# Performance work log

Measured on AMD Instinct MI355X. Metric: run time of the kernel, lower is better.

Reference implementation:

```python
import jax, jax.numpy as jnp
import numpy as np
import math

NUM_SECTORS = 8
HIDDEN = 128
FEAT = 64
MAX_DIST = 10.0


def gru_last(x, Wih, Whh, bih, bhh):
    # PyTorch GRU (gate order r,z,n); x: (B,T,D) -> last hidden (B,H)
    B = x.shape[0]
    H = Whh.shape[1]
    xp = jnp.einsum('btd,gd->btg', x, Wih) + bih  # (B,T,3H)

    def step(h, xpt):
        hp = h @ Whh.T + bhh
        xr, xz, xn = jnp.split(xpt, 3, -1)
        hr, hz, hn = jnp.split(hp, 3, -1)
        r = jax.nn.sigmoid(xr + hr)
        z = jax.nn.sigmoid(xz + hz)
        n = jnp.tanh(xn + r * hn)
        h_new = (1.0 - z) * n + z * h
        return h_new, None

    h0 = jnp.zeros((B, H), x.dtype)
    hT, _ = jax.lax.scan(step, h0, jnp.swapaxes(xp, 0, 1))
    return hT


def setup_inputs() -> dict:
    key = jax.random.key(0)
    ks = iter(jax.random.split(key, 32))
    B, N, T = 2048, 64, 8
    H, Hn = HIDDEN, HIDDEN // 2
    s = 0.05

    def p(shape):
        return jax.random.normal(next(ks), shape, jnp.float32) * s

    inp = {
        'target_trajectory': jax.random.normal(next(ks), (B, T, 2), jnp.float32),
        'neighbor_trajectories': jax.random.normal(next(ks), (B, N, T, 2), jnp.float32),
        'relative_angles': jax.random.uniform(next(ks), (B, N), jnp.float32) * (2.0 * math.pi),
        'neighbor_mask': (jax.random.uniform(next(ks), (B, N)) > 0.2).astype(jnp.float32),
        # target GRU (H=128)
        'Wih_t': p((3 * H, 2)), 'Whh_t': p((3 * H, H)), 'bih_t': p((3 * H,)), 'bhh_t': p((3 * H,)),
        # neighbor GRU (H=64)
        'Wih_n': p((3 * Hn, 2)), 'Whh_n': p((3 * Hn, Hn)), 'bih_n': p((3 * Hn,)), 'bhh_n': p((3 * Hn,)),
        # sector encoder: 68 -> 128 -> 128
        'W1': p((H, 4 + Hn)), 'b1': p((H,)), 'W2': p((H, H)), 'b2': p((H,)),
        # fusion: 1152 -> 256 -> 128 -> 64
        'Wf1': p((2 * H, H + NUM_SECTORS * H)), 'bf1': p((2 * H,)),
        'Wf2': p((H, 2 * H)), 'bf2': p((H,)),
        'Wf3': p((FEAT, H)), 'bf3': p((FEAT,)),
        'ln_g': jnp.ones((FEAT,), jnp.float32), 'ln_b': jnp.zeros((FEAT,), jnp.float32),
    }
    return inp


def reference(target_trajectory, neighbor_trajectories, relative_angles, neighbor_mask,
              Wih_t, Whh_t, bih_t, bhh_t, Wih_n, Whh_n, bih_n, bhh_n,
              W1, b1, W2, b2, Wf1, bf1, Wf2, bf2, Wf3, bf3, ln_g, ln_b):
    B, N, T, D = neighbor_trajectories.shape
    S = NUM_SECTORS

    # trajectory encoders
    target_feature = gru_last(target_trajectory, Wih_t, Whh_t, bih_t, bhh_t)  # (B,128)
    nf = gru_last(neighbor_trajectories.reshape(B * N, T, D), Wih_n, Whh_n, bih_n, bhh_n)
    nf = nf.reshape(B, N, -1)  # (B,N,64)

    # geometry
    target_pos = target_trajectory[:, -1, :]                      # (B,2)
    npos = neighbor_trajectories[:, :, -1, :]                     # (B,N,2)
    dist = jnp.linalg.norm(npos - target_pos[:, None, :], axis=-1)  # (B,N)
    vel = neighbor_trajectories[:, :, -1, :] - neighbor_trajectories[:, :, -2, :]  # (B,N,2)

    # sector assignment (vectorized segment reduce over sectors)
    sector_size = 2.0 * math.pi / S
    sid = jnp.clip((relative_angles / sector_size).astype(jnp.int32), 0, S - 1)  # (B,N)
    valid = neighbor_mask > 0
    memb = ((sid[..., None] == jnp.arange(S)) & valid[..., None]).astype(dist.dtype)  # (B,N,S)

    count = memb.sum(1)                        # (B,S)
    nonempty = count > 0
    safe = jnp.maximum(count, 1.0)
    avg_d = jnp.where(nonempty, (dist[..., None] * memb).sum(1) / safe, 0.0)  # (B,S)
    avg_v = jnp.where(nonempty[..., None], jnp.einsum('bns,bnc->bsc', memb, vel) / safe[..., None], 0.0)

    w = jnp.exp(-dist / MAX_DIST)              # (B,N)
    wm = w[..., None] * memb                   # (B,N,S)
    wsum = wm.sum(1) + 1e-8                    # (B,S)
    wfeat = jnp.einsum('bns,bnh->bsh', wm, nf) / wsum[..., None]  # (B,S,64)

    sector_feats = jnp.concatenate([count[..., None], avg_d[..., None], avg_v, wfeat], axis=-1)  # (B,S,68)

    # sector encoder MLP (dropout off / eval)
    h = jax.nn.relu(sector_feats @ W1.T + b1)
    h = jax.nn.relu(h @ W2.T + b2)             # (B,S,128)
    enc = h.reshape(B, S * HIDDEN)

    combined = jnp.concatenate([target_feature, enc], axis=-1)  # (B,1152)
    f = jax.nn.relu(combined @ Wf1.T + bf1)
    f = jax.nn.relu(f @ Wf2.T + bf2)
    f = jax.nn.relu(f @ Wf3.T + bf3)           # (B,64)

    mu = f.mean(-1, keepdims=True)
    var = ((f - mu) ** 2).mean(-1, keepdims=True)
    return (f - mu) / jnp.sqrt(var + 1e-5) * ln_g + ln_b
```

## Files before the change

kernel.cpp:

```cpp
#include <hip/hip_runtime.h>

typedef __attribute__((ext_vector_type(8))) short short8;
typedef __attribute__((ext_vector_type(4))) float f32x4;

__device__ __forceinline__ unsigned short f2bf(float f){
  unsigned u = __float_as_uint(f);
  return (unsigned short)((u + 0x7fffu + ((u >> 16) & 1u)) >> 16);
}
__device__ __forceinline__ float bf2f(unsigned short b){
  return __uint_as_float(((unsigned)b) << 16);
}
__device__ __forceinline__ float sigf(float v){
  return __builtin_amdgcn_rcpf(1.0f + __builtin_amdgcn_exp2f(v * -1.44269504088896341f));
}
__device__ __forceinline__ float tanhf_fast(float v){
  float e = __builtin_amdgcn_exp2f(v * 2.88539008177792681f);
  return (e - 1.0f) * __builtin_amdgcn_rcpf(e + 1.0f);
}

__global__ __launch_bounds__(256) void k_prep(
    const float* __restrict__ Whh_t, const float* __restrict__ W1,
    const float* __restrict__ W2,    const float* __restrict__ Wf1,
    const float* __restrict__ Wf2,   const float* __restrict__ Wf3,
    const float* __restrict__ Whh_n,
    unsigned short* __restrict__ wgt)
{
  int i = blockIdx.x * 256 + threadIdx.x;
  if (i < 49152){ wgt[i] = f2bf(Whh_t[i]); return; }
  i -= 49152;
  if (i < 12288){ int r = i / 96, c = i % 96;
    wgt[49152 + i] = (c < 68) ? f2bf(W1[r*68 + c]) : (unsigned short)0; return; }
  i -= 12288;
  if (i < 16384){ wgt[61440 + i] = f2bf(W2[i]); return; }
  i -= 16384;
  if (i < 294912){ wgt[77824 + i] = f2bf(Wf1[i]); return; }
  i -= 294912;
  if (i < 32768){ wgt[372736 + i] = f2bf(Wf2[i]); return; }
  i -= 32768;
  if (i < 8192){ wgt[405504 + i] = f2bf(Wf3[i]); return; }
  i -= 8192;
  if (i < 12288){ wgt[413696 + i] = f2bf(Whh_n[i]); return; }
}

__global__ __launch_bounds__(512, 4) void k_gru_n(
    const float* __restrict__ ttraj, const float* __restrict__ ntraj,
    const float* __restrict__ rang,  const float* __restrict__ nmask,
    const float* __restrict__ Wih_n,
    const float* __restrict__ bih_n, const float* __restrict__ bhh_n,
    const unsigned short* __restrict__ wgt,
    unsigned short* __restrict__ sf)
{
  __shared__ char smem[60928];
  const int tid = threadIdx.x;
  const int bi = tid >> 8, lt = tid & 255;
  const int w = lt >> 6, u = (lt >> 4) & 3, c = lt & 15;
  const int b = blockIdx.x * 2 + bi;
  const unsigned short* whhN_b = wgt + 413696;

  unsigned short* whh  = (unsigned short*)smem;
  char* pb = smem + 27648 + bi * 16640;
  unsigned short* hall = (unsigned short*)pb;
  unsigned short* hb   = hall + w * 1152;
  float* xs   = (float*)(pb + 9216);
  float* wm   = (float*)(pb + 13312);
  float* dv   = (float*)(pb + 15360);
  float* sidv = (float*)(pb + 16128);
  float* sect = (float*)(pb + 16384);

  for (int i = tid; i < 1536; i += 512){
    int r = i >> 3, cg = (i & 7) * 8;
    *(short8*)&whh[r*72 + cg] = *(const short8*)&whhN_b[r*64 + cg];
  }
  ((float4*)xs)[lt] = ((const float4*)(ntraj + (size_t)b * 1024))[lt];
  wm[lt] = 0.0f; wm[256 + lt] = 0.0f;
  __syncthreads();

  float wr0[4],wr1[4],br_[4],wz0[4],wz1[4],bz_[4],wn0[4],wn1[4],bi_[4],bh_[4];
#pragma unroll
  for (int gt = 0; gt < 4; ++gt){
    int g = gt*16 + c;
    wr0[gt]=Wih_n[g*2];  wr1[gt]=Wih_n[g*2+1];  br_[gt]=bih_n[g]+bhh_n[g];
    int gz = 64+g;  wz0[gt]=Wih_n[gz*2]; wz1[gt]=Wih_n[gz*2+1]; bz_[gt]=bih_n[gz]+bhh_n[gz];
    int gn = 128+g; wn0[gt]=Wih_n[gn*2]; wn1[gt]=Wih_n[gn*2+1]; bi_[gt]=bih_n[gn]; bh_[gt]=bhh_n[gn];
  }
  float hcur[4][4];
#pragma unroll
  for (int gt=0; gt<4; ++gt)
#pragma unroll
    for (int q=0; q<4; ++q) hcur[gt][q] = 0.0f;

  for (int st = 0; st < 8; ++st){
    f32x4 acc[12];
    if (st > 0){
      short8 a0 = *(short8*)&hb[c*72 + u*8];
      short8 a1 = *(short8*)&hb[c*72 + 32 + u*8];
#pragma unroll
      for (int nt = 0; nt < 12; ++nt){
        short8 b0 = *(short8*)&whh[(nt*16+c)*72 + u*8];
        short8 b1 = *(short8*)&whh[(nt*16+c)*72 + 32 + u*8];
        f32x4 t = {0.f,0.f,0.f,0.f};
        t = __builtin_amdgcn_mfma_f32_16x16x32_bf16(a0, b0, t, 0,0,0);
        acc[nt] = __builtin_amdgcn_mfma_f32_16x16x32_bf16(a1, b1, t, 0,0,0);
      }
    } else {
#pragma unroll
      for (int nt = 0; nt < 12; ++nt) acc[nt] = (f32x4){0.f,0.f,0.f,0.f};
    }
    float xq0[4], xq1[4];
#pragma unroll
    for (int q=0; q<4; ++q){
      int sq = w*16 + u*4 + q;
      xq0[q] = xs[sq*16 + st*2];
      xq1[q] = xs[sq*16 + st*2 + 1];
    }
#pragma unroll
    for (int gt=0; gt<4; ++gt){
#pragma unroll
      for (int q=0; q<4; ++q){
        float x0 = xq0[q], x1 = xq1[q];
        float rp = wr0[gt]*x0 + wr1[gt]*x1 + br_[gt] + acc[gt][q];
        float zp = wz0[gt]*x0 + wz1[gt]*x1 + bz_[gt] + acc[4+gt][q];
        float r = sigf(rp), z = sigf(zp);
        float hn = acc[8+gt][q] + bh_[gt];
        float pn = wn0[gt]*x0 + wn1[gt]*x1 + bi_[gt] + r*hn;
        float n = tanhf_fast(pn);
        float hnew = n + z*(hcur[gt][q] - n);
        hcur[gt][q] = hnew;
        hb[(u*4+q)*72 + gt*16 + c] = f2bf(hnew);
      }
    }
  }
  __syncthreads();

  if (lt < 64){
    int n = lt;
    float m   = nmask[(size_t)b*64 + n];
    float ang = rang[(size_t)b*64 + n];
    float tx = ttraj[(size_t)b*16 + 14], ty = ttraj[(size_t)b*16 + 15];
    float px = xs[n*16+14], py = xs[n*16+15];
    float vx = px - xs[n*16+12], vy = py - xs[n*16+13];
    float dx = px - tx, dy = py - ty;
    float dist = __builtin_amdgcn_sqrtf(dx*dx + dy*dy);
    int sid = (int)(ang / 0.78539816339744830962f);
    sid = sid < 0 ? 0 : (sid > 7 ? 7 : sid);
    bool valid = m > 0.0f;
    float wv = valid ? __builtin_amdgcn_exp2f(dist * -0.14426950408889634f) : 0.0f;
    wm[n*8 + sid] = wv;
    dv[n]      = valid ? dist : 0.0f;
    dv[64+n]   = valid ? vx   : 0.0f;
    dv[128+n]  = valid ? vy   : 0.0f;
    sidv[n]    = valid ? (float)sid : -1.0f;
  }
  __syncthreads();
  if (lt < 8){
    int s = lt;
    float cnt=0.f, sd=0.f, sx=0.f, sy=0.f, sw=0.f;
    for (int n=0; n<64; ++n){
      if (sidv[n] == (float)s){
        cnt += 1.f; sd += dv[n]; sx += dv[64+n]; sy += dv[128+n]; sw += wm[n*8+s];
      }
    }
    float inv = (cnt > 0.f) ? __builtin_amdgcn_rcpf(cnt) : 0.f;
    sect[s*8+0] = cnt;
    sect[s*8+1] = sd * inv;
    sect[s*8+2] = sx * inv;
    sect[s*8+3] = sy * inv;
    sect[s*8+4] = __builtin_amdgcn_rcpf(sw + 1e-8f);
  }
  __syncthreads();
#pragma unroll
  for (int rep = 0; rep < 2; ++rep){
    int p = lt + rep*256;
    int s = p >> 6, h = p & 63;
    float a = 0.f;
    for (int n = 0; n < 64; ++n){
      float wmv = wm[n*8 + s];
      float nf  = bf2f(hall[(n>>4)*1152 + (n&15)*72 + h]);
      a += wmv * nf;
    }
    sf[((size_t)b*8 + s)*96 + 4 + h] = f2bf(a * sect[s*8+4]);
  }
  if (lt < 32){
    int s = lt >> 2, cc = lt & 3;
    sf[((size_t)b*8 + s)*96 + cc] = f2bf(sect[s*8+cc]);
  }
  if (lt < 224){
    int s = lt / 28, cc = 68 + lt % 28;
    sf[((size_t)b*8 + s)*96 + cc] = 0;
  }
}

__global__ __launch_bounds__(256) void k_gru_t(
    const float* __restrict__ ttraj,
    const float* __restrict__ Wih_t, const float* __restrict__ bih_t, const float* __restrict__ bhh_t,
    const unsigned short* __restrict__ wgt,
    unsigned short* __restrict__ combined)
{
  __shared__ char smem[9728];
  const int tid = threadIdx.x, w = tid >> 6, u = (tid >> 4) & 3, c = tid & 15;
  unsigned short* hb0 = (unsigned short*)smem;
  unsigned short* hb1 = (unsigned short*)(smem + 4352);
  float* xs = (float*)(smem + 8704);

  xs[tid] = ttraj[(size_t)blockIdx.x*256 + tid];

  int ntg[6];
  ntg[0] = 2*w; ntg[1] = 2*w+1;
  ntg[2] = 8+2*w; ntg[3] = 9+2*w;
  ntg[4] = 16+2*w; ntg[5] = 17+2*w;

  short8 Bf[6][4];
#pragma unroll
  for (int lt2 = 0; lt2 < 6; ++lt2){
    const unsigned short* wp = wgt + (ntg[lt2]*16 + c)*128 + u*8;
#pragma unroll
    for (int kk = 0; kk < 4; ++kk)
      Bf[lt2][kk] = *(const short8*)(wp + kk*32);
  }

  float Wr0[2],Wr1[2],BR[2],Wz0[2],Wz1[2],BZ[2],Wn0[2],Wn1[2],BI[2],BH[2];
#pragma unroll
  for (int gt = 0; gt < 2; ++gt){
    int g = w*32 + gt*16 + c;
    Wr0[gt]=Wih_t[g*2];        Wr1[gt]=Wih_t[g*2+1];        BR[gt]=bih_t[g]+bhh_t[g];
    Wz0[gt]=Wih_t[(128+g)*2];  Wz1[gt]=Wih_t[(128+g)*2+1];  BZ[gt]=bih_t[128+g]+bhh_t[128+g];
    Wn0[gt]=Wih_t[(256+g)*2];  Wn1[gt]=Wih_t[(256+g)*2+1];  BI[gt]=bih_t[256+g]; BH[gt]=bhh_t[256+g];
  }
  float hcur[2][4];
#pragma unroll
  for (int gt=0; gt<2; ++gt)
#pragma unroll
    for (int q=0; q<4; ++q) hcur[gt][q] = 0.0f;
  __syncthreads();

  for (int st = 0; st < 8; ++st){
    unsigned short* rbuf = (st & 1) ? hb0 : hb1;
    unsigned short* wbuf = (st & 1) ? hb1 : hb0;
    f32x4 acc[6];
    if (st > 0){
      short8 a0 = *(short8*)&rbuf[c*136 + u*8];
      short8 a1 = *(short8*)&rbuf[c*136 + 32 + u*8];
      short8 a2 = *(short8*)&rbuf[c*136 + 64 + u*8];
      short8 a3 = *(short8*)&rbuf[c*136 + 96 + u*8];
#pragma unroll
      for (int lt2 = 0; lt2 < 6; ++lt2){
        f32x4 t = {0.f,0.f,0.f,0.f};
        t = __builtin_amdgcn_mfma_f32_16x16x32_bf16(a0, Bf[lt2][0], t, 0,0,0);
        t = __builtin_amdgcn_mfma_f32_16x16x32_bf16(a1, Bf[lt2][1], t, 0,0,0);
        t = __builtin_amdgcn_mfma_f32_16x16x32_bf16(a2, Bf[lt2][2], t, 0,0,0);
        acc[lt2] = __builtin_amdgcn_mfma_f32_16x16x32_bf16(a3, Bf[lt2][3], t, 0,0,0);
      }
    } else {
#pragma unroll
      for (int lt2 = 0; lt2 < 6; ++lt2) acc[lt2] = (f32x4){0.f,0.f,0.f,0.f};
    }
#pragma unroll
    for (int gt = 0; gt < 2; ++gt){
#pragma unroll
      for (int q = 0; q < 4; ++q){
        int sq = u*4 + q;
        float x0 = xs[sq*16 + st*2], x1 = xs[sq*16 + st*2 + 1];
        float rp = Wr0[gt]*x0 + Wr1[gt]*x1 + BR[gt] + acc[gt][q];
        float zp = Wz0[gt]*x0 + Wz1[gt]*x1 + BZ[gt] + acc[2+gt][q];
        float r = sigf(rp), z = sigf(zp);
        float hn = acc[4+gt][q] + BH[gt];
        float pn = Wn0[gt]*x0 + Wn1[gt]*x1 + BI[gt] + r*hn;
        float n = tanhf_fast(pn);
        float hnew = n + z*(hcur[gt][q] - n);
        hcur[gt][q] = hnew;
        if (st < 7){
          wbuf[sq*136 + w*32 + gt*16 + c] = f2bf(hnew);
        } else {
          int row = blockIdx.x*16 + sq;
          combined[(size_t)row*1152 + w*32 + gt*16 + c] = f2bf(hnew);
        }
      }
    }
    if (st < 7) __syncthreads();
  }
}

__global__ __launch_bounds__(256) void k_mlp12(
    const unsigned short* __restrict__ sf,
    const unsigned short* __restrict__ wgt,
    const float* __restrict__ b1, const float* __restrict__ b2,
    unsigned short* __restrict__ combined)
{
  __shared__ char smem[18432];
  unsigned short* hb = (unsigned short*)smem + (threadIdx.x >> 6) * 2176;
  float* b1s = (float*)(smem + 17408);
  float* b2s = b1s + 128;
  const unsigned short* w1b = wgt + 49152;
  const unsigned short* w2b = wgt + 61440;
  const int tid = threadIdx.x, w = tid >> 6, u = (tid >> 4) & 3, c = tid & 15;
  if (tid < 128){ b1s[tid] = b1[tid]; b2s[tid] = b2[tid]; }
  __syncthreads();
  const int rowb = blockIdx.x * 64 + w * 16;

  f32x4 acc[8];
#pragma unroll
  for (int nt=0; nt<8; ++nt) acc[nt] = (f32x4){0.f,0.f,0.f,0.f};
#pragma unroll
  for (int kc=0; kc<3; ++kc){
    short8 a = *(const short8*)&sf[(size_t)(rowb + c)*96 + kc*32 + u*8];
#pragma unroll
    for (int nt=0; nt<8; ++nt){
      short8 bb = *(const short8*)&w1b[(nt*16+c)*96 + kc*32 + u*8];
      acc[nt] = __builtin_amdgcn_mfma_f32_16x16x32_bf16(a, bb, acc[nt], 0,0,0);
    }
  }
#pragma unroll
  for (int nt=0; nt<8; ++nt){
    float bias = b1s[nt*16+c];
#pragma unroll
    for (int q=0; q<4; ++q){
      float v = acc[nt][q] + bias; v = v > 0.f ? v : 0.f;
      hb[(u*4+q)*136 + nt*16 + c] = f2bf(v);
    }
  }
  f32x4 acc2[8];
#pragma unroll
  for (int nt=0; nt<8; ++nt) acc2[nt] = (f32x4){0.f,0.f,0.f,0.f};
#pragma unroll
  for (int kc=0; kc<4; ++kc){
    short8 a = *(short8*)&hb[c*136 + kc*32 + u*8];
#pragma unroll
    for (int nt=0; nt<8; ++nt){
      short8 bb = *(const short8*)&w2b[(nt*16+c)*128 + kc*32 + u*8];
      acc2[nt] = __builtin_amdgcn_mfma_f32_16x16x32_bf16(a, bb, acc2[nt], 0,0,0);
    }
  }
#pragma unroll
  for (int nt=0; nt<8; ++nt){
    float bias = b2s[nt*16+c];
#pragma unroll
    for (int q=0; q<4; ++q){
      float v = acc2[nt][q] + bias; v = v > 0.f ? v : 0.f;
      int r = rowb + u*4 + q;
      combined[(size_t)(r >> 3)*1152 + 128 + (r & 7)*128 + nt*16 + c] = f2bf(v);
    }
  }
}

__global__ __launch_bounds__(256) void k_head(
    const unsigned short* __restrict__ combined,
    const unsigned short* __restrict__ wgt,
    const float* __restrict__ bf1, const float* __restrict__ bf2, const float* __restrict__ bf3,
    const float* __restrict__ lng, const float* __restrict__ lnb,
    float* __restrict__ out)
{
  __shared__ char smem[15104];
  const int tid = threadIdx.x, w = tid >> 6, u = (tid >> 4) & 3, c = tid & 15;
  unsigned short* f1b = (unsigned short*)smem;
  unsigned short* f2b = (unsigned short*)(smem + 8448);
  float* bf1s = (float*)(smem + 12800); float* bf2s = (float*)(smem + 13824);
  float* bf3s = (float*)(smem + 14336);
  float* lngs = (float*)(smem + 14592); float* lnbs = (float*)(smem + 14848);
  const unsigned short* wf1b = wgt + 77824;
  const unsigned short* wf2b = wgt + 372736;
  const unsigned short* wf3b = wgt + 405504;
  bf1s[tid] = bf1[tid];
  if (tid < 128) bf2s[tid] = bf2[tid];
  if (tid < 64){ bf3s[tid] = bf3[tid]; lngs[tid] = lng[tid]; lnbs[tid] = lnb[tid]; }
  __syncthreads();
  const int rowb = blockIdx.x * 16;

  f32x4 acc[4];
#pragma unroll
  for (int i=0; i<4; ++i) acc[i] = (f32x4){0.f,0.f,0.f,0.f};
#pragma unroll 4
  for (int kc=0; kc<36; ++kc){
    short8 a = *(const short8*)&combined[(size_t)(rowb + c)*1152 + kc*32 + u*8];
#pragma unroll
    for (int i=0; i<4; ++i){
      int nt = w*4 + i;
      short8 bb = *(const short8*)&wf1b[(size_t)(nt*16+c)*1152 + kc*32 + u*8];
      acc[i] = __builtin_amdgcn_mfma_f32_16x16x32_bf16(a, bb, acc[i], 0,0,0);
    }
  }
#pragma unroll
  for (int i=0; i<4; ++i){
    int nt = w*4 + i;
    float bias = bf1s[nt*16+c];
#pragma unroll
    for (int q=0; q<4; ++q){
      float v = acc[i][q] + bias; v = v > 0.f ? v : 0.f;
      f1b[(u*4+q)*264 + nt*16 + c] = f2bf(v);
    }
  }
  __syncthreads();

  f32x4 acc2[2];
#pragma unroll
  for (int i=0; i<2; ++i) acc2[i] = (f32x4){0.f,0.f,0.f,0.f};
#pragma unroll
  for (int kc=0; kc<8; ++kc){
    short8 a = *(short8*)&f1b[c*264 + kc*32 + u*8];
#pragma unroll
    for (int i=0; i<2; ++i){
      int nt = w*2 + i;
      short8 bb = *(const short8*)&wf2b[(nt*16+c)*256 + kc*32 + u*8];
      acc2[i] = __builtin_amdgcn_mfma_f32_16x16x32_bf16(a, bb, acc2[i], 0,0,0);
    }
  }
#pragma unroll
  for (int i=0; i<2; ++i){
    int nt = w*2 + i;
    float bias = bf2s[nt*16+c];
#pragma unroll
    for (int q=0; q<4; ++q){
      float v = acc2[i][q] + bias; v = v > 0.f ? v : 0.f;
      f2b[(u*4+q)*136 + nt*16 + c] = f2bf(v);
    }
  }
  __syncthreads();

  f32x4 acc3[4];
#pragma unroll
  for (int nt=0; nt<4; ++nt) acc3[nt] = (f32x4){0.f,0.f,0.f,0.f};
#pragma unroll
  for (int kc=0; kc<4; ++kc){
    short8 a = *(short8*)&f2b[c*136 + kc*32 + u*8];
#pragma unroll
    for (int nt=0; nt<4; ++nt){
      short8 bb = *(const short8*)&wf3b[(nt*16+c)*128 + kc*32 + u*8];
      acc3[nt] = __builtin_amdgcn_mfma_f32_16x16x32_bf16(a, bb, acc3[nt], 0,0,0);
    }
  }
  if (w == 0){
    float v[4][4];
#pragma unroll
    for (int nt=0; nt<4; ++nt){
      float bias = bf3s[nt*16+c];
#pragma unroll
      for (int q=0; q<4; ++q){
        float t = acc3[nt][q] + bias; v[nt][q] = t > 0.f ? t : 0.f;
      }
    }
#pragma unroll
    for (int q=0; q<4; ++q){
      float p = v[0][q] + v[1][q] + v[2][q] + v[3][q];
      p += __shfl_xor(p, 1); p += __shfl_xor(p, 2); p += __shfl_xor(p, 4); p += __shfl_xor(p, 8);
      float mu = p * 0.015625f;
      float d0 = v[0][q]-mu, d1 = v[1][q]-mu, d2 = v[2][q]-mu, d3 = v[3][q]-mu;
      float p2 = d0*d0 + d1*d1 + d2*d2 + d3*d3;
      p2 += __shfl_xor(p2, 1); p2 += __shfl_xor(p2, 2); p2 += __shfl_xor(p2, 4); p2 += __shfl_xor(p2, 8);
      float rstd = __builtin_amdgcn_rsqf(p2 * 0.015625f + 1e-5f);
      int row = rowb + u*4 + q;
#pragma unroll
      for (int nt=0; nt<4; ++nt){
        int col = nt*16 + c;
        out[(size_t)row*64 + col] = (v[nt][q] - mu) * rstd * lngs[col] + lnbs[col];
      }
    }
  }
}

extern "C" void kernel_launch(void* const* d_in, const int* in_sizes, int n_in,
                              void* d_out, int out_size, void* d_ws, size_t ws_size,
                              hipStream_t stream)
{
  const float* ttraj = (const float*)d_in[0];
  const float* ntraj = (const float*)d_in[1];
  const float* rang  = (const float*)d_in[2];
  const float* nmask = (const float*)d_in[3];
  const float* Wih_t = (const float*)d_in[4];
  const float* Whh_t = (const float*)d_in[5];
  const float* bih_t = (const float*)d_in[6];
  const float* bhh_t = (const float*)d_in[7];
  const float* Wih_n = (const float*)d_in[8];
  const float* Whh_n = (const float*)d_in[9];
  const float* bih_n = (const float*)d_in[10];
  const float* bhh_n = (const float*)d_in[11];
  const float* W1  = (const float*)d_in[12];
  const float* b1  = (const float*)d_in[13];
  const float* W2  = (const float*)d_in[14];
  const float* b2  = (const float*)d_in[15];
  const float* Wf1 = (const float*)d_in[16];
  const float* bf1 = (const float*)d_in[17];
  const float* Wf2 = (const float*)d_in[18];
  const float* bf2 = (const float*)d_in[19];
  const float* Wf3 = (const float*)d_in[20];
  const float* bf3 = (const float*)d_in[21];
  const float* lng = (const float*)d_in[22];
  const float* lnb = (const float*)d_in[23];

  char* ws = (char*)d_ws;
  unsigned short* combined = (unsigned short*)ws;
  unsigned short* sf       = (unsigned short*)(ws + 5242880);
  unsigned short* wgt      = (unsigned short*)(ws + 8388608);

  hipLaunchKernelGGL(k_prep, dim3(1664), dim3(256), 0, stream,
                     Whh_t, W1, W2, Wf1, Wf2, Wf3, Whh_n, wgt);
  hipLaunchKernelGGL(k_gru_n, dim3(1024), dim3(512), 0, stream,
                     ttraj, ntraj, rang, nmask, Wih_n, bih_n, bhh_n, wgt, sf);
  hipLaunchKernelGGL(k_gru_t, dim3(128), dim3(256), 0, stream,
                     ttraj, Wih_t, bih_t, bhh_t, wgt, combined);
  hipLaunchKernelGGL(k_mlp12, dim3(256), dim3(256), 0, stream, sf, wgt, b1, b2, combined);
  hipLaunchKernelGGL(k_head, dim3(128), dim3(256), 0, stream,
                     combined, wgt, bf1, bf2, bf3, lng, lnb, (float*)d_out);
}
```

Measured before the change: 150.5 us.

## Fold gate exp2 scales into weights, use hardware bf16 convert, interleave GRU MFMA

Pre-scales the recurrent and input GRU weights and biases by the log2e-based constants so the sigmoid and tanh become a bare exp2 plus reciprocal, with FMA-fused gate math. Replaces the software round-to-nearest bf16 conversion with the v_cvt_pk_bf16_f32 instruction everywhere. In the neighbor GRU, MFMAs are issued per gate tile with the gate math interleaved, which lowers accumulator register pressure. The trajectory smem rows are padded to 20 floats with float2 loads. Scaling the weights before bf16 rounding changes the rounding slightly, and the inline asm ties the code to the gfx950 ISA.

```diff
diff --git a/kernel.cpp b/kernel.cpp
--- a/kernel.cpp
+++ b/kernel.cpp
@@ -2,6 +2,9 @@
 
 typedef __attribute__((ext_vector_type(8))) short short8;
 typedef __attribute__((ext_vector_type(4))) float f32x4;
+
+#define SGC (-1.44269504088896341f)
+#define THC ( 2.88539008177792681f)
 
 __device__ __forceinline__ unsigned short f2bf(float f){
   unsigned u = __float_as_uint(f);
@@ -10,12 +13,10 @@
 __device__ __forceinline__ float bf2f(unsigned short b){
   return __uint_as_float(((unsigned)b) << 16);
 }
-__device__ __forceinline__ float sigf(float v){
-  return __builtin_amdgcn_rcpf(1.0f + __builtin_amdgcn_exp2f(v * -1.44269504088896341f));
-}
-__device__ __forceinline__ float tanhf_fast(float v){
-  float e = __builtin_amdgcn_exp2f(v * 2.88539008177792681f);
-  return (e - 1.0f) * __builtin_amdgcn_rcpf(e + 1.0f);
+__device__ __forceinline__ unsigned f2bf_cvt(float f){
+  unsigned r;
+  asm("v_cvt_pk_bf16_f32 %0, %1, %1" : "=v"(r) : "v"(f));
+  return r;
 }
 
 __global__ __launch_bounds__(256) void k_prep(
@@ -26,7 +27,11 @@
     unsigned short* __restrict__ wgt)
 {
   int i = blockIdx.x * 256 + threadIdx.x;
-  if (i < 49152){ wgt[i] = f2bf(Whh_t[i]); return; }
+  if (i < 49152){
+    int g = i >> 7;
+    float s = (g < 256) ? SGC : THC;
+    wgt[i] = f2bf(Whh_t[i] * s); return;
+  }
   i -= 49152;
   if (i < 12288){ int r = i / 96, c = i % 96;
     wgt[49152 + i] = (c < 68) ? f2bf(W1[r*68 + c]) : (unsigned short)0; return; }
@@ -39,7 +44,11 @@
   i -= 32768;
   if (i < 8192){ wgt[405504 + i] = f2bf(Wf3[i]); return; }
   i -= 8192;
-  if (i < 12288){ wgt[413696 + i] = f2bf(Whh_n[i]); return; }
+  if (i < 12288){
+    int g = i >> 6;
+    float s = (g < 128) ? SGC : THC;
+    wgt[413696 + i] = f2bf(Whh_n[i] * s); return;
+  }
 }
 
 __global__ __launch_bounds__(512, 4) void k_gru_n(
@@ -50,7 +59,7 @@
     const unsigned short* __restrict__ wgt,
     unsigned short* __restrict__ sf)
 {
-  __shared__ char smem[60928];
+  __shared__ char smem[62976];
   const int tid = threadIdx.x;
   const int bi = tid >> 8, lt = tid & 255;
   const int w = lt >> 6, u = (lt >> 4) & 3, c = lt & 15;
@@ -58,20 +67,23 @@
   const unsigned short* whhN_b = wgt + 413696;
 
   unsigned short* whh  = (unsigned short*)smem;
-  char* pb = smem + 27648 + bi * 16640;
+  char* pb = smem + 27648 + bi * 17664;
   unsigned short* hall = (unsigned short*)pb;
   unsigned short* hb   = hall + w * 1152;
   float* xs   = (float*)(pb + 9216);
-  float* wm   = (float*)(pb + 13312);
-  float* dv   = (float*)(pb + 15360);
-  float* sidv = (float*)(pb + 16128);
-  float* sect = (float*)(pb + 16384);
+  float* wm   = (float*)(pb + 14336);
+  float* dv   = (float*)(pb + 16384);
+  float* sidv = (float*)(pb + 17152);
+  float* sect = (float*)(pb + 17408);
 
   for (int i = tid; i < 1536; i += 512){
     int r = i >> 3, cg = (i & 7) * 8;
     *(short8*)&whh[r*72 + cg] = *(const short8*)&whhN_b[r*64 + cg];
   }
-  ((float4*)xs)[lt] = ((const float4*)(ntraj + (size_t)b * 1024))[lt];
+  {
+    int row = lt >> 2, part = lt & 3;
+    *(float4*)&xs[row*20 + part*4] = ((const float4*)(ntraj + (size_t)b * 1024))[lt];
+  }
   wm[lt] = 0.0f; wm[256 + lt] = 0.0f;
   __syncthreads();
 
@@ -79,9 +91,9 @@
 #pragma unroll
   for (int gt = 0; gt < 4; ++gt){
     int g = gt*16 + c;
-    wr0[gt]=Wih_n[g*2];  wr1[gt]=Wih_n[g*2+1];  br_[gt]=bih_n[g]+bhh_n[g];
-    int gz = 64+g;  wz0[gt]=Wih_n[gz*2]; wz1[gt]=Wih_n[gz*2+1]; bz_[gt]=bih_n[gz]+bhh_n[gz];
-    int gn = 128+g; wn0[gt]=Wih_n[gn*2]; wn1[gt]=Wih_n[gn*2+1]; bi_[gt]=bih_n[gn]; bh_[gt]=bhh_n[gn];
+    wr0[gt]=Wih_n[g*2]*SGC;  wr1[gt]=Wih_n[g*2+1]*SGC;  br_[gt]=(bih_n[g]+bhh_n[g])*SGC;
+    int gz = 64+g;  wz0[gt]=Wih_n[gz*2]*SGC; wz1[gt]=Wih_n[gz*2+1]*SGC; bz_[gt]=(bih_n[gz]+bhh_n[gz])*SGC;
+    int gn = 128+g; wn0[gt]=Wih_n[gn*2]*THC; wn1[gt]=Wih_n[gn*2+1]*THC; bi_[gt]=bih_n[gn]*THC; bh_[gt]=bhh_n[gn]*THC;
   }
   float hcur[4][4];
 #pragma unroll
@@ -89,45 +101,52 @@
 #pragma unroll
     for (int q=0; q<4; ++q) hcur[gt][q] = 0.0f;
 
+  float xq0[4], xq1[4];
+  auto gates = [&](int gt, const f32x4& aR, const f32x4& aZ, const f32x4& aN){
+#pragma unroll
+    for (int q = 0; q < 4; ++q){
+      float x0 = xq0[q], x1 = xq1[q];
+      float rp = __builtin_fmaf(wr0[gt], x0, __builtin_fmaf(wr1[gt], x1, aR[q] + br_[gt]));
+      float zp = __builtin_fmaf(wz0[gt], x0, __builtin_fmaf(wz1[gt], x1, aZ[q] + bz_[gt]));
+      float r = __builtin_amdgcn_rcpf(1.0f + __builtin_amdgcn_exp2f(rp));
+      float z = __builtin_amdgcn_rcpf(1.0f + __builtin_amdgcn_exp2f(zp));
+      float hnv = aN[q] + bh_[gt];
+      float pn = __builtin_fmaf(wn0[gt], x0, __builtin_fmaf(wn1[gt], x1, __builtin_fmaf(r, hnv, bi_[gt])));
+      float E = __builtin_amdgcn_exp2f(pn);
+      float n = __builtin_fmaf(-2.0f, __builtin_amdgcn_rcpf(E + 1.0f), 1.0f);
+      float hnew = __builtin_fmaf(z, hcur[gt][q] - n, n);
+      hcur[gt][q] = hnew;
+      hb[(u*4+q)*72 + gt*16 + c] = (unsigned short)f2bf_cvt(hnew);
+    }
+  };
+
   for (int st = 0; st < 8; ++st){
-    f32x4 acc[12];
+#pragma unroll
+    for (int q=0; q<4; ++q){
+      float2 xv = *(const float2*)&xs[(w*16 + u*4 + q)*20 + st*2];
+      xq0[q] = xv.x; xq1[q] = xv.y;
+    }
     if (st > 0){
       short8 a0 = *(short8*)&hb[c*72 + u*8];
       short8 a1 = *(short8*)&hb[c*72 + 32 + u*8];
-#pragma unroll
-      for (int nt = 0; nt < 12; ++nt){
-        short8 b0 = *(short8*)&whh[(nt*16+c)*72 + u*8];
-        short8 b1 = *(short8*)&whh[(nt*16+c)*72 + 32 + u*8];
-        f32x4 t = {0.f,0.f,0.f,0.f};
-        t = __builtin_amdgcn_mfma_f32_16x16x32_bf16(a0, b0, t, 0,0,0);
-        acc[nt] = __builtin_amdgcn_mfma_f32_16x16x32_bf16(a1, b1, t, 0,0,0);
+      f32x4 zz = {0.f,0.f,0.f,0.f};
+#pragma unroll
+      for (int gt = 0; gt < 4; ++gt){
+        const unsigned short* pr = &whh[(gt*16+c)*72 + u*8];
+        const unsigned short* pz = &whh[((4+gt)*16+c)*72 + u*8];
+        const unsigned short* pq = &whh[((8+gt)*16+c)*72 + u*8];
+        f32x4 aR = __builtin_amdgcn_mfma_f32_16x16x32_bf16(a0, *(const short8*)pr, zz, 0,0,0);
+        aR = __builtin_amdgcn_mfma_f32_16x16x32_bf16(a1, *(const short8*)(pr+32), aR, 0,0,0);
+        f32x4 aZ = __builtin_amdgcn_mfma_f32_16x16x32_bf16(a0, *(const short8*)pz, zz, 0,0,0);
+        aZ = __builtin_amdgcn_mfma_f32_16x16x32_bf16(a1, *(const short8*)(pz+32), aZ, 0,0,0);
+        f32x4 aN = __builtin_amdgcn_mfma_f32_16x16x32_bf16(a0, *(const short8*)pq, zz, 0,0,0);
+        aN = __builtin_amdgcn_mfma_f32_16x16x32_bf16(a1, *(const short8*)(pq+32), aN, 0,0,0);
+        gates(gt, aR, aZ, aN);
       }
     } else {
-#pragma unroll
-      for (int nt = 0; nt < 12; ++nt) acc[nt] = (f32x4){0.f,0.f,0.f,0.f};
-    }
-    float xq0[4], xq1[4];
-#pragma unroll
-    for (int q=0; q<4; ++q){
-      int sq = w*16 + u*4 + q;
-      xq0[q] = xs[sq*16 + st*2];
-      xq1[q] = xs[sq*16 + st*2 + 1];
-    }
-#pragma unroll
-    for (int gt=0; gt<4; ++gt){
-#pragma unroll
-      for (int q=0; q<4; ++q){
-        float x0 = xq0[q], x1 = xq1[q];
-        float rp = wr0[gt]*x0 + wr1[gt]*x1 + br_[gt] + acc[gt][q];
-        float zp = wz0[gt]*x0 + wz1[gt]*x1 + bz_[gt] + acc[4+gt][q];
-        float r = sigf(rp), z = sigf(zp);
-        float hn = acc[8+gt][q] + bh_[gt];
-        float pn = wn0[gt]*x0 + wn1[gt]*x1 + bi_[gt] + r*hn;
-        float n = tanhf_fast(pn);
-        float hnew = n + z*(hcur[gt][q] - n);
-        hcur[gt][q] = hnew;
-        hb[(u*4+q)*72 + gt*16 + c] = f2bf(hnew);
-      }
+      f32x4 zz = {0.f,0.f,0.f,0.f};
+#pragma unroll
+      for (int gt = 0; gt < 4; ++gt) gates(gt, zz, zz, zz);
     }
   }
   __syncthreads();
@@ -137,8 +156,8 @@
     float m   = nmask[(size_t)b*64 + n];
     float ang = rang[(size_t)b*64 + n];
     float tx = ttraj[(size_t)b*16 + 14], ty = ttraj[(size_t)b*16 + 15];
-    float px = xs[n*16+14], py = xs[n*16+15];
-    float vx = px - xs[n*16+12], vy = py - xs[n*16+13];
+    float px = xs[n*20+14], py = xs[n*20+15];
+    float vx = px - xs[n*20+12], vy = py - xs[n*20+13];
     float dx = px - tx, dy = py - ty;
     float dist = __builtin_amdgcn_sqrtf(dx*dx + dy*dy);
     int sid = (int)(ang / 0.78539816339744830962f);
@@ -178,11 +197,11 @@
       float nf  = bf2f(hall[(n>>4)*1152 + (n&15)*72 + h]);
       a += wmv * nf;
     }
-    sf[((size_t)b*8 + s)*96 + 4 + h] = f2bf(a * sect[s*8+4]);
+    sf[((size_t)b*8 + s)*96 + 4 + h] = (unsigned short)f2bf_cvt(a * sect[s*8+4]);
   }
   if (lt < 32){
     int s = lt >> 2, cc = lt & 3;
-    sf[((size_t)b*8 + s)*96 + cc] = f2bf(sect[s*8+cc]);
+    sf[((size_t)b*8 + s)*96 + cc] = (unsigned short)f2bf_cvt(sect[s*8+cc]);
   }
   if (lt < 224){
     int s = lt / 28, cc = 68 + lt % 28;
@@ -222,9 +241,9 @@
 #pragma unroll
   for (int gt = 0; gt < 2; ++gt){
     int g = w*32 + gt*16 + c;
-    Wr0[gt]=Wih_t[g*2];        Wr1[gt]=Wih_t[g*2+1];        BR[gt]=bih_t[g]+bhh_t[g];
-    Wz0[gt]=Wih_t[(128+g)*2];  Wz1[gt]=Wih_t[(128+g)*2+1];  BZ[gt]=bih_t[128+g]+bhh_t[128+g];
-    Wn0[gt]=Wih_t[(256+g)*2];  Wn1[gt]=Wih_t[(256+g)*2+1];  BI[gt]=bih_t[256+g]; BH[gt]=bhh_t[256+g];
+    Wr0[gt]=Wih_t[g*2]*SGC;        Wr1[gt]=Wih_t[g*2+1]*SGC;        BR[gt]=(bih_t[g]+bhh_t[g])*SGC;
+    Wz0[gt]=Wih_t[(128+g)*2]*SGC;  Wz1[gt]=Wih_t[(128+g)*2+1]*SGC;  BZ[gt]=(bih_t[128+g]+bhh_t[128+g])*SGC;
+    Wn0[gt]=Wih_t[(256+g)*2]*THC;  Wn1[gt]=Wih_t[(256+g)*2+1]*THC;  BI[gt]=bih_t[256+g]*THC; BH[gt]=bhh_t[256+g]*THC;
   }
   float hcur[2][4];
 #pragma unroll
@@ -260,19 +279,21 @@
       for (int q = 0; q < 4; ++q){
         int sq = u*4 + q;
         float x0 = xs[sq*16 + st*2], x1 = xs[sq*16 + st*2 + 1];
-        float rp = Wr0[gt]*x0 + Wr1[gt]*x1 + BR[gt] + acc[gt][q];
-        float zp = Wz0[gt]*x0 + Wz1[gt]*x1 + BZ[gt] + acc[2+gt][q];
-        float r = sigf(rp), z = sigf(zp);
-        float hn = acc[4+gt][q] + BH[gt];
-        float pn = Wn0[gt]*x0 + Wn1[gt]*x1 + BI[gt] + r*hn;
-        float n = tanhf_fast(pn);
-        float hnew = n + z*(hcur[gt][q] - n);
+        float rp = __builtin_fmaf(Wr0[gt], x0, __builtin_fmaf(Wr1[gt], x1, acc[gt][q] + BR[gt]));
+        float zp = __builtin_fmaf(Wz0[gt], x0, __builtin_fmaf(Wz1[gt], x1, acc[2+gt][q] + BZ[gt]));
+        float r = __builtin_amdgcn_rcpf(1.0f + __builtin_amdgcn_exp2f(rp));
+        float z = __builtin_amdgcn_rcpf(1.0f + __builtin_amdgcn_exp2f(zp));
+        float hnv = acc[4+gt][q] + BH[gt];
+        float pn = __builtin_fmaf(Wn0[gt], x0, __builtin_fmaf(Wn1[gt], x1, __builtin_fmaf(r, hnv, BI[gt])));
+        float E = __builtin_amdgcn_exp2f(pn);
+        float n = __builtin_fmaf(-2.0f, __builtin_amdgcn_rcpf(E + 1.0f), 1.0f);
+        float hnew = __builtin_fmaf(z, hcur[gt][q] - n, n);
         hcur[gt][q] = hnew;
         if (st < 7){
-          wbuf[sq*136 + w*32 + gt*16 + c] = f2bf(hnew);
+          wbuf[sq*136 + w*32 + gt*16 + c] = (unsigned short)f2bf_cvt(hnew);
         } else {
           int row = blockIdx.x*16 + sq;
-          combined[(size_t)row*1152 + w*32 + gt*16 + c] = f2bf(hnew);
+          combined[(size_t)row*1152 + w*32 + gt*16 + c] = (unsigned short)f2bf_cvt(hnew);
         }
       }
     }
@@ -315,7 +336,7 @@
 #pragma unroll
     for (int q=0; q<4; ++q){
       float v = acc[nt][q] + bias; v = v > 0.f ? v : 0.f;
-      hb[(u*4+q)*136 + nt*16 + c] = f2bf(v);
+      hb[(u*4+q)*136 + nt*16 + c] = (unsigned short)f2bf_cvt(v);
     }
   }
   f32x4 acc2[8];
@@ -337,7 +358,7 @@
     for (int q=0; q<4; ++q){
       float v = acc2[nt][q] + bias; v = v > 0.f ? v : 0.f;
       int r = rowb + u*4 + q;
-      combined[(size_t)(r >> 3)*1152 + 128 + (r & 7)*128 + nt*16 + c] = f2bf(v);
+      combined[(size_t)(r >> 3)*1152 + 128 + (r & 7)*128 + nt*16 + c] = (unsigned short)f2bf_cvt(v);
     }
   }
 }
@@ -385,7 +406,7 @@
 #pragma unroll
     for (int q=0; q<4; ++q){
       float v = acc[i][q] + bias; v = v > 0.f ? v : 0.f;
-      f1b[(u*4+q)*264 + nt*16 + c] = f2bf(v);
+      f1b[(u*4+q)*264 + nt*16 + c] = (unsigned short)f2bf_cvt(v);
     }
   }
   __syncthreads();
@@ -410,7 +431,7 @@
 #pragma unroll
     for (int q=0; q<4; ++q){
       float v = acc2[i][q] + bias; v = v > 0.f ? v : 0.f;
-      f2b[(u*4+q)*136 + nt*16 + c] = f2bf(v);
+      f2b[(u*4+q)*136 + nt*16 + c] = (unsigned short)f2bf_cvt(v);
     }
   }
   __syncthreads();
```

After: 136.6 us. 1.1x faster.
